# Optimization experiments

Measured on AMD Instinct MI355X. Metric: run time of the kernel, lower is better.

The kernel has to match this reference:

```python
import jax, jax.numpy as jnp
import numpy as np

N_NODES = 50000
N_EDGES = 800000
IN_F = 512
H_F = 32
HEADS = 8
N_CLS = 40
NEG_SLOPE = 0.2


def gat_conv(h, W, al, ar, b, src, dst, n_heads, d_out):
    """DGL-style GATConv. h: [N, F_in]; W: [F_in, n_heads*d_out];
    al, ar: [n_heads, d_out]; b: [n_heads*d_out]. Returns [N, n_heads, d_out]."""
    n = h.shape[0]
    feat = (h @ W).reshape(n, n_heads, d_out)            # [N, H, D]
    el = jnp.sum(feat * al[None], axis=-1)               # [N, H]
    er = jnp.sum(feat * ar[None], axis=-1)               # [N, H]
    e = jax.nn.leaky_relu(el[src] + er[dst], NEG_SLOPE)  # [E, H]
    # numerically stable edge softmax per destination node
    m = jax.ops.segment_max(e, dst, num_segments=n)      # [N, H]
    m = jnp.where(jnp.isfinite(m), m, 0.0)
    ee = jnp.exp(e - m[dst])                             # [E, H]
    den = jax.ops.segment_sum(ee, dst, num_segments=n)   # [N, H]
    alpha = ee / jnp.maximum(den[dst], 1e-9)             # [E, H]
    msg = alpha[:, :, None] * feat[src]                  # [E, H, D]
    rst = jax.ops.segment_sum(msg, dst, num_segments=n)  # [N, H, D]
    return rst + b.reshape(1, n_heads, d_out)


def setup_inputs() -> dict:
    key = jax.random.key(0)
    ks = jax.random.split(key, 16)
    hid = H_F * HEADS
    s = lambda fan: 1.0 / np.sqrt(fan)
    return {
        "in_feat": jax.random.normal(ks[0], (N_NODES, IN_F), jnp.float32),
        "src": jax.random.randint(ks[1], (N_EDGES,), 0, N_NODES, jnp.int32),
        "dst": jax.random.randint(ks[2], (N_EDGES,), 0, N_NODES, jnp.int32),
        "W0": jax.random.normal(ks[3], (IN_F, hid), jnp.float32) * s(IN_F),
        "al0": jax.random.normal(ks[4], (HEADS, H_F), jnp.float32) * s(H_F),
        "ar0": jax.random.normal(ks[5], (HEADS, H_F), jnp.float32) * s(H_F),
        "b0": jnp.zeros((hid,), jnp.float32),
        "W1": jax.random.normal(ks[6], (hid, hid), jnp.float32) * s(hid),
        "al1": jax.random.normal(ks[7], (HEADS, H_F), jnp.float32) * s(H_F),
        "ar1": jax.random.normal(ks[8], (HEADS, H_F), jnp.float32) * s(H_F),
        "b1": jnp.zeros((hid,), jnp.float32),
        "W2": jax.random.normal(ks[9], (hid, N_CLS), jnp.float32) * s(hid),
        "al2": jax.random.normal(ks[10], (1, N_CLS), jnp.float32) * s(N_CLS),
        "ar2": jax.random.normal(ks[11], (1, N_CLS), jnp.float32) * s(N_CLS),
        "b2": jnp.zeros((N_CLS,), jnp.float32),
    }


def reference(in_feat, src, dst, W0, al0, ar0, b0, W1, al1, ar1, b1,
              W2, al2, ar2, b2):
    n = in_feat.shape[0]
    # layer 0 + ReLU (dropout p=0.0 is identity) + flatten heads
    h = gat_conv(in_feat, W0, al0, ar0, b0, src, dst, HEADS, H_F)
    h = jax.nn.relu(h).reshape(n, -1)
    # layer 1
    h = gat_conv(h, W1, al1, ar1, b1, src, dst, HEADS, H_F)
    h = jax.nn.relu(h).reshape(n, -1)
    # output layer, single head, no activation
    h = gat_conv(h, W2, al2, ar2, b2, src, dst, 1, N_CLS)
    return h.reshape(n, -1)
```

## Files before the change

kernel.cpp:

```cpp
#include <hip/hip_runtime.h>
#include <hip/hip_bf16.h>

#define N_NODES 50000
#define N_EDGES 800000
#define IN_F 512
#define HID 256
#define HEADS 8
#define DHEAD 32
#define N_CLS 40
#define NCLS_PAD 64

typedef __bf16 bf16x8 __attribute__((ext_vector_type(8)));
typedef float f32x4 __attribute__((ext_vector_type(4)));

#define AT_AL0 0
#define AT_AR0 256
#define AT_AL1 512
#define AT_AR1 768
#define AT_AL2 1024
#define AT_AR2 1088
#define AT_B0  1152
#define AT_B1  1408
#define AT_B2  1664
#define AT_SZ  1792

__device__ __forceinline__ float ldflag(const void* p, long long i, int isbf) {
  return isbf ? __bfloat162float(((const __hip_bfloat16*)p)[i])
              : ((const float*)p)[i];
}
__device__ __forceinline__ float blo(unsigned u) { return __uint_as_float(u << 16); }
__device__ __forceinline__ float bhi(unsigned u) { return __uint_as_float(u & 0xffff0000u); }
__device__ __forceinline__ unsigned pk2(float a, float b) {
  unsigned x = __bfloat16_as_ushort(__float2bfloat16(a));
  unsigned y = __bfloat16_as_ushort(__float2bfloat16(b));
  return x | (y << 16);
}
__device__ __forceinline__ void gload16(const unsigned short* g, unsigned short* l) {
  __builtin_amdgcn_global_load_lds((__attribute__((address_space(1))) void*)g,
                                   (__attribute__((address_space(3))) void*)l, 16, 0, 0);
}

__global__ void k_zero(int* __restrict__ cursor) {
  int i = blockIdx.x * blockDim.x + threadIdx.x;
  if (i < N_NODES) cursor[i] = 0;
}

__global__ void k_detect_prep(const unsigned short* __restrict__ raw, int* __restrict__ flag,
                              const void* al0, const void* ar0, const void* al1, const void* ar1,
                              const void* al2, const void* ar2, const void* b0, const void* b1,
                              const void* b2, float* __restrict__ att) {
  __shared__ int cnt[256];
  int t = threadIdx.x;
  int c = 0;
  for (int i = t; i < 8192; i += 256) {
    int e = (raw[i] >> 7) & 0xFF;
    if (e >= 0x90) c++;
  }
  cnt[t] = c;
  __syncthreads();
  for (int s = 128; s; s >>= 1) {
    if (t < s) cnt[t] += cnt[t + s];
    __syncthreads();
  }
  __shared__ int sflag;
  if (t == 0) { sflag = (cnt[0] > 64) ? 0 : 1; *flag = sflag; }
  __syncthreads();
  int isbf = sflag;
  att[AT_AL0 + t] = ldflag(al0, t, isbf);
  att[AT_AR0 + t] = ldflag(ar0, t, isbf);
  att[AT_AL1 + t] = ldflag(al1, t, isbf);
  att[AT_AR1 + t] = ldflag(ar1, t, isbf);
  att[AT_B0 + t]  = ldflag(b0, t, isbf);
  att[AT_B1 + t]  = ldflag(b1, t, isbf);
  if (t < N_CLS) {
    att[AT_AL2 + t] = ldflag(al2, t, isbf);
    att[AT_AR2 + t] = ldflag(ar2, t, isbf);
    att[AT_B2 + t]  = ldflag(b2, t, isbf);
  }
}

__global__ void k_hist(const int* __restrict__ dst, int* __restrict__ cnt) {
  int e = blockIdx.x * blockDim.x + threadIdx.x;
  if (e < N_EDGES) atomicAdd(&cnt[dst[e]], 1);
}

#define SCAN_B 512
#define SCAN_NB ((N_NODES + SCAN_B - 1) / SCAN_B)

__global__ __launch_bounds__(SCAN_B) void k_scan_blocks(const int* __restrict__ deg,
                                                        int* __restrict__ excl,
                                                        int* __restrict__ partial) {
  __shared__ int buf[SCAN_B];
  int t = threadIdx.x;
  int i = blockIdx.x * SCAN_B + t;
  int v = (i < N_NODES) ? deg[i] : 0;
  buf[t] = v;
  __syncthreads();
  for (int off = 1; off < SCAN_B; off <<= 1) {
    int x = (t >= off) ? buf[t - off] : 0;
    __syncthreads();
    buf[t] += x;
    __syncthreads();
  }
  if (i < N_NODES) excl[i] = buf[t] - v;
  if (t == SCAN_B - 1) partial[blockIdx.x] = buf[t];
}

__global__ void k_scan_partials(int* __restrict__ partial, int* __restrict__ rowptr) {
  __shared__ int buf[SCAN_NB];
  int t = threadIdx.x;
  if (t < SCAN_NB) buf[t] = partial[t];
  __syncthreads();
  if (t == 0) {
    int run = 0;
    for (int b = 0; b < SCAN_NB; b++) { int v = buf[b]; buf[b] = run; run += v; }
    rowptr[N_NODES] = run;
  }
  __syncthreads();
  if (t < SCAN_NB) partial[t] = buf[t];
}

__global__ void k_scan_add(int* __restrict__ rowptr, const int* __restrict__ partial,
                           int* __restrict__ cursor) {
  int i = blockIdx.x * blockDim.x + threadIdx.x;
  if (i < N_NODES) {
    rowptr[i] += partial[i / SCAN_B];
    cursor[i] = 0;
  }
}

__global__ void k_scatter(const int* __restrict__ src, const int* __restrict__ dst,
                          const int* __restrict__ rowptr, int* __restrict__ cursor,
                          int* __restrict__ csr_src) {
  int e = blockIdx.x * blockDim.x + threadIdx.x;
  if (e < N_EDGES) {
    int d = dst[e];
    int pos = rowptr[d] + atomicAdd(&cursor[d], 1);
    csr_src[pos] = src[e];
  }
}

#define TW0 (HID * IN_F)
#define TW1 (TW0 + HID * HID)
#define TW2 (TW1 + NCLS_PAD * HID)
__global__ void k_transpose_all(const void* __restrict__ W0, const void* __restrict__ W1,
                                const void* __restrict__ W2,
                                __hip_bfloat16* __restrict__ w0t, __hip_bfloat16* __restrict__ w1t,
                                __hip_bfloat16* __restrict__ w2t, const int* __restrict__ flag) {
  int isbf = *flag;
  int i = blockIdx.x * blockDim.x + threadIdx.x;
  if (i < TW0) {
    int n = i >> 9, k = i & 511;
    w0t[i] = __float2bfloat16(ldflag(W0, (long long)k * HID + n, isbf));
  } else if (i < TW1) {
    int j = i - TW0;
    int n = j >> 8, k = j & 255;
    w1t[j] = __float2bfloat16(ldflag(W1, (long long)k * HID + n, isbf));
  } else if (i < TW2) {
    int j = i - TW1;
    int n = j >> 8, k = j & 255;
    float v = (n < N_CLS) ? ldflag(W2, (long long)k * N_CLS + n, isbf) : 0.f;
    w2t[j] = __float2bfloat16(v);
  }
}

__global__ __launch_bounds__(256, 8) void k_gemm64hi(const void* __restrict__ A,
                                                     const __hip_bfloat16* __restrict__ Bt,
                                                     __hip_bfloat16* __restrict__ C,
                                                     int M, int K, int N, int ldc, int nvalid,
                                                     const int* __restrict__ flag, int force_bf,
                                                     const float* __restrict__ al,
                                                     const float* __restrict__ ar,
                                                     float* __restrict__ el,
                                                     float* __restrict__ er, int fuse_eler) {
  __shared__ unsigned short sA[64 * 64];
  __shared__ unsigned short sB[64 * 64];
  const int isbf = force_bf ? 1 : *flag;
  int nwg = gridDim.x;
  int q = nwg >> 3, r = nwg & 7;
  int xcd = blockIdx.x & 7, lid = blockIdx.x >> 3;
  int logical = (xcd < r ? xcd * (q + 1) : r * (q + 1) + (xcd - r) * q) + lid;
  int nblk = N >> 6;
  int mb = logical / nblk;
  int nb = logical - mb * nblk;
  int m0 = mb << 6, n0 = nb << 6;
  int tid = threadIdx.x;
  int lane = tid & 63, wave = tid >> 6;
  int wm = (wave >> 1) << 5, wn = (wave & 1) << 5;
  int lm = lane & 15, quad = lane >> 4;
  int rbase = tid >> 3;
  int srcoff = ((tid & 7) ^ (rbase & 7)) << 3;
  const unsigned short* Ab = (const unsigned short*)A;
  const float* Af = (const float*)A;
  const unsigned short* Bb = (const unsigned short*)Bt;
  size_t abase[2];
  size_t bbase[2];
  #pragma unroll
  for (int i = 0; i < 2; i++) {
    int row = (i << 5) + rbase;
    int ga = m0 + row; if (ga > M - 1) ga = M - 1;
    abase[i] = (size_t)ga * K + srcoff;
    bbase[i] = (size_t)(n0 + row) * K + srcoff;
  }
  f32x4 acc[2][2] = {};
  int nph = K >> 6;
  for (int p = 0; p < nph; ++p) {
    int kph = p << 6;
    if (isbf) {
      #pragma unroll
      for (int i = 0; i < 2; i++) {
        gload16(Ab + abase[i] + kph, &sA[(((i << 8) + tid) << 3)]);
        gload16(Bb + bbase[i] + kph, &sB[(((i << 8) + tid) << 3)]);
      }
    } else {
      #pragma unroll
      for (int i = 0; i < 2; i++) {
        gload16(Bb + bbase[i] + kph, &sB[(((i << 8) + tid) << 3)]);
        const float* p0 = Af + abase[i] + kph;
        float4 x = *(const float4*)p0;
        float4 y = *(const float4*)(p0 + 4);
        *(uint4*)&sA[(((i << 8) + tid) << 3)] =
            make_uint4(pk2(x.x, x.y), pk2(x.z, x.w), pk2(y.x, y.y), pk2(y.z, y.w));
      }
    }
    __syncthreads();
    #pragma unroll
    for (int s = 0; s < 2; s++) {
      bf16x8 af[2], bfr[2];
      #pragma unroll
      for (int i = 0; i < 2; i++) {
        int ra = wm + (i << 4) + lm;
        int rb = wn + (i << 4) + lm;
        int sl = (((s << 2) + quad) ^ (lm & 7)) << 3;
        af[i]  = *(const bf16x8*)&sA[(ra << 6) + sl];
        bfr[i] = *(const bf16x8*)&sB[(rb << 6) + sl];
      }
      #pragma unroll
      for (int mi = 0; mi < 2; mi++)
        #pragma unroll
        for (int ni = 0; ni < 2; ni++)
          acc[mi][ni] = __builtin_amdgcn_mfma_f32_16x16x32_bf16(af[mi], bfr[ni], acc[mi][ni], 0, 0, 0);
    }
    __syncthreads();
  }
  #pragma unroll
  for (int mi = 0; mi < 2; mi++)
    #pragma unroll
    for (int ni = 0; ni < 2; ni++)
      #pragma unroll
      for (int r2 = 0; r2 < 4; r2++) {
        int gm = m0 + wm + mi * 16 + (quad << 2) + r2;
        int gn = n0 + wn + ni * 16 + lm;
        if (gm < M && gn < nvalid) C[(size_t)gm * ldc + gn] = __float2bfloat16(acc[mi][ni][r2]);
      }
  if (fuse_eler) {
    int hg = (n0 + wn) >> 5;
    float ala[2], ara[2];
    #pragma unroll
    for (int ni = 0; ni < 2; ni++) {
      ala[ni] = al[hg * DHEAD + ni * 16 + lm];
      ara[ni] = ar[hg * DHEAD + ni * 16 + lm];
    }
    #pragma unroll
    for (int mi = 0; mi < 2; mi++)
      #pragma unroll
      for (int r2 = 0; r2 < 4; r2++) {
        float pl = acc[mi][0][r2] * ala[0] + acc[mi][1][r2] * ala[1];
        float pr = acc[mi][0][r2] * ara[0] + acc[mi][1][r2] * ara[1];
        #pragma unroll
        for (int d = 1; d < 16; d <<= 1) {
          pl += __shfl_xor(pl, d, 16);
          pr += __shfl_xor(pr, d, 16);
        }
        int gm = m0 + wm + mi * 16 + (quad << 2) + r2;
        if (lm == 0 && gm < M) {
          el[gm * HEADS + hg] = pl;
          er[gm * HEADS + hg] = pr;
        }
      }
  }
}

__global__ void k_eler2(const __hip_bfloat16* __restrict__ feat2,
                        const float* __restrict__ al, const float* __restrict__ ar,
                        float* __restrict__ el, float* __restrict__ er) {
  int n = blockIdx.x * blockDim.x + threadIdx.x;
  if (n >= N_NODES) return;
  const __hip_bfloat16* f = feat2 + (size_t)n * N_CLS;
  float sl = 0.f, sr = 0.f;
  for (int d = 0; d < N_CLS; d++) {
    float v = __bfloat162float(f[d]);
    sl += v * al[d];
    sr += v * ar[d];
  }
  el[n] = sl;
  er[n] = sr;
}

__global__ __launch_bounds__(256) void k_aggregate8(const int* __restrict__ rowptr,
                                                    const int* __restrict__ csr_src,
                                                    const uint4* __restrict__ feat_rows,
                                                    const float* __restrict__ el,
                                                    const float* __restrict__ er,
                                                    const float* __restrict__ bias,
                                                    __hip_bfloat16* __restrict__ out) {
  __shared__ float lds_acc[8][256];
  __shared__ float lds_l[8][32];
  int n = blockIdx.x;
  int t = threadIdx.x;
  int slot = t >> 5;
  int c = t & 31;
  int hh = c >> 2;
  float er_n = er[n * HEADS + hh];
  int beg = rowptr[n], end = rowptr[n + 1];
  float l = 0.f;
  float acc[8] = {0.f, 0.f, 0.f, 0.f, 0.f, 0.f, 0.f, 0.f};
  int i = beg + slot;
  for (; i + 8 < end; i += 16) {
    int s1 = csr_src[i];
    int s2 = csr_src[i + 8];
    float el1 = el[s1 * HEADS + hh];
    float el2 = el[s2 * HEADS + hh];
    uint4 f1 = feat_rows[(size_t)s1 * 32 + c];
    uint4 f2 = feat_rows[(size_t)s2 * 32 + c];
    float x1 = el1 + er_n, x2 = el2 + er_n;
    float e1 = x1 > 0.f ? x1 : 0.2f * x1;
    float e2 = x2 > 0.f ? x2 : 0.2f * x2;
    float p1 = __expf(fminf(e1, 60.f));
    float p2 = __expf(fminf(e2, 60.f));
    l += p1 + p2;
    acc[0] += p1 * blo(f1.x) + p2 * blo(f2.x); acc[1] += p1 * bhi(f1.x) + p2 * bhi(f2.x);
    acc[2] += p1 * blo(f1.y) + p2 * blo(f2.y); acc[3] += p1 * bhi(f1.y) + p2 * bhi(f2.y);
    acc[4] += p1 * blo(f1.z) + p2 * blo(f2.z); acc[5] += p1 * bhi(f1.z) + p2 * bhi(f2.z);
    acc[6] += p1 * blo(f1.w) + p2 * blo(f2.w); acc[7] += p1 * bhi(f1.w) + p2 * bhi(f2.w);
  }
  if (i < end) {
    int s = csr_src[i];
    float elv = el[s * HEADS + hh];
    uint4 fv = feat_rows[(size_t)s * 32 + c];
    float x = elv + er_n;
    float e = x > 0.f ? x : 0.2f * x;
    float p = __expf(fminf(e, 60.f));
    l += p;
    acc[0] += p * blo(fv.x); acc[1] += p * bhi(fv.x);
    acc[2] += p * blo(fv.y); acc[3] += p * bhi(fv.y);
    acc[4] += p * blo(fv.z); acc[5] += p * bhi(fv.z);
    acc[6] += p * blo(fv.w); acc[7] += p * bhi(fv.w);
  }
  *(float4*)&lds_acc[slot][c * 8]     = make_float4(acc[0], acc[1], acc[2], acc[3]);
  *(float4*)&lds_acc[slot][c * 8 + 4] = make_float4(acc[4], acc[5], acc[6], acc[7]);
  lds_l[slot][c] = l;
  __syncthreads();
  float a = 0.f, L = 0.f;
  #pragma unroll
  for (int s2 = 0; s2 < 8; s2++) { a += lds_acc[s2][t]; L += lds_l[s2][t >> 3]; }
  float o = a / fmaxf(L, 1e-9f) + bias[t];
  o = fmaxf(o, 0.f);
  out[(size_t)n * HID + t] = __float2bfloat16(o);
}

__global__ __launch_bounds__(256) void k_aggregate1(const int* __restrict__ rowptr,
                                                    const int* __restrict__ csr_src,
                                                    const char* __restrict__ fr2,
                                                    const float* __restrict__ el,
                                                    const float* __restrict__ er,
                                                    const float* __restrict__ bias,
                                                    void* __restrict__ out,
                                                    const int* __restrict__ flag) {
  __shared__ float lds_acc[32][64];
  __shared__ float lds_l[32][8];
  int isbf = *flag;
  int n = blockIdx.x;
  int t = threadIdx.x;
  int slot = t >> 3;
  int c = t & 7;
  int beg = rowptr[n], end = rowptr[n + 1];
  if (c < 5) {
    float er_n = er[n];
    float l = 0.f;
    float acc[8] = {0.f, 0.f, 0.f, 0.f, 0.f, 0.f, 0.f, 0.f};
    unsigned cb = (unsigned)c << 4;
    int i = beg + slot;
    for (; i + 32 < end; i += 64) {
      int s1 = csr_src[i], s2 = csr_src[i + 32];
      float el1 = el[s1], el2 = el[s2];
      uint4 f1 = *(const uint4*)(fr2 + (unsigned)s1 * 80u + cb);
      uint4 f2 = *(const uint4*)(fr2 + (unsigned)s2 * 80u + cb);
      float x1 = el1 + er_n, x2 = el2 + er_n;
      float e1 = x1 > 0.f ? x1 : 0.2f * x1;
      float e2 = x2 > 0.f ? x2 : 0.2f * x2;
      float p1 = __expf(fminf(e1, 60.f));
      float p2 = __expf(fminf(e2, 60.f));
      l += p1 + p2;
      acc[0] += p1 * blo(f1.x) + p2 * blo(f2.x); acc[1] += p1 * bhi(f1.x) + p2 * bhi(f2.x);
      acc[2] += p1 * blo(f1.y) + p2 * blo(f2.y); acc[3] += p1 * bhi(f1.y) + p2 * bhi(f2.y);
      acc[4] += p1 * blo(f1.z) + p2 * blo(f2.z); acc[5] += p1 * bhi(f1.z) + p2 * bhi(f2.z);
      acc[6] += p1 * blo(f1.w) + p2 * blo(f2.w); acc[7] += p1 * bhi(f1.w) + p2 * bhi(f2.w);
    }
    if (i < end) {
      int s = csr_src[i];
      float x = el[s] + er_n;
      uint4 fv = *(const uint4*)(fr2 + (unsigned)s * 80u + cb);
      float e = x > 0.f ? x : 0.2f * x;
      float p = __expf(fminf(e, 60.f));
      l += p;
      acc[0] += p * blo(fv.x); acc[1] += p * bhi(fv.x);
      acc[2] += p * blo(fv.y); acc[3] += p * bhi(fv.y);
      acc[4] += p * blo(fv.z); acc[5] += p * bhi(fv.z);
      acc[6] += p * blo(fv.w); acc[7] += p * bhi(fv.w);
    }
    *(float4*)&lds_acc[slot][c * 8]     = make_float4(acc[0], acc[1], acc[2], acc[3]);
    *(float4*)&lds_acc[slot][c * 8 + 4] = make_float4(acc[4], acc[5], acc[6], acc[7]);
    lds_l[slot][c] = l;
  }
  __syncthreads();
  if (t < N_CLS) {
    float a = 0.f, L = 0.f;
    #pragma unroll
    for (int s2 = 0; s2 < 32; s2++) { a += lds_acc[s2][t]; L += lds_l[s2][t >> 3]; }
    float o = a / fmaxf(L, 1e-9f) + bias[t];
    if (isbf) ((__hip_bfloat16*)out)[(size_t)n * N_CLS + t] = __float2bfloat16(o);
    else      ((float*)out)[(size_t)n * N_CLS + t] = o;
  }
}

static inline size_t align_up(size_t x) { return (x + 255) & ~(size_t)255; }

extern "C" void kernel_launch(void* const* d_in, const int* in_sizes, int n_in,
                              void* d_out, int out_size, void* d_ws, size_t ws_size,
                              hipStream_t stream) {
  const void* in_feat = d_in[0];
  const int* src = (const int*)d_in[1];
  const int* dst = (const int*)d_in[2];
  const void* W0  = d_in[3];
  const void* al0 = d_in[4];
  const void* ar0 = d_in[5];
  const void* b0  = d_in[6];
  const void* W1  = d_in[7];
  const void* al1 = d_in[8];
  const void* ar1 = d_in[9];
  const void* b1  = d_in[10];
  const void* W2  = d_in[11];
  const void* al2 = d_in[12];
  const void* ar2 = d_in[13];
  const void* b2  = d_in[14];

  char* p = (char*)d_ws;
  int* flag = (int*)p;                   p += 256;
  float* att = (float*)p;                p += align_up(AT_SZ * sizeof(float));
  int* rowptr = (int*)p;                 p += align_up((N_NODES + 1) * sizeof(int));
  int* cursor = (int*)p;                 p += align_up(N_NODES * sizeof(int));
  int* csr_src = (int*)p;                p += align_up(N_EDGES * sizeof(int));
  int* partial = (int*)p;                p += align_up(SCAN_NB * sizeof(int));
  __hip_bfloat16* feat16 = (__hip_bfloat16*)p; p += align_up((size_t)N_NODES * HID * sizeof(__hip_bfloat16));
  __hip_bfloat16* h16 = (__hip_bfloat16*)p;    p += align_up((size_t)N_NODES * HID * sizeof(__hip_bfloat16));
  float* el = (float*)p;                 p += align_up((size_t)N_NODES * HEADS * sizeof(float));
  float* er = (float*)p;                 p += align_up((size_t)N_NODES * HEADS * sizeof(float));
  __hip_bfloat16* w0t = (__hip_bfloat16*)p;    p += align_up((size_t)HID * IN_F * sizeof(__hip_bfloat16));
  __hip_bfloat16* w1t = (__hip_bfloat16*)p;    p += align_up((size_t)HID * HID * sizeof(__hip_bfloat16));
  __hip_bfloat16* w2t = (__hip_bfloat16*)p;    p += align_up((size_t)NCLS_PAD * HID * sizeof(__hip_bfloat16));

  const int EB = (N_EDGES + 255) / 256;
  const int NB256 = (N_NODES + 255) / 256;
  const int MB64 = (N_NODES + 63) / 64;
  const int GXL = MB64 * 4;
  const int GX2 = MB64;

  k_detect_prep<<<1, 256, 0, stream>>>((const unsigned short*)in_feat, flag,
                                       al0, ar0, al1, ar1, al2, ar2, b0, b1, b2, att);
  k_zero<<<NB256, 256, 0, stream>>>(cursor);

  k_hist<<<EB, 256, 0, stream>>>(dst, cursor);
  k_scan_blocks<<<SCAN_NB, SCAN_B, 0, stream>>>(cursor, rowptr, partial);
  k_scan_partials<<<1, 128, 0, stream>>>(partial, rowptr);
  k_scan_add<<<NB256, 256, 0, stream>>>(rowptr, partial, cursor);
  k_scatter<<<EB, 256, 0, stream>>>(src, dst, rowptr, cursor, csr_src);

  k_transpose_all<<<(TW2 + 255) / 256, 256, 0, stream>>>(W0, W1, W2, w0t, w1t, w2t, flag);

  k_gemm64hi<<<GXL, 256, 0, stream>>>(in_feat, w0t, feat16, N_NODES, IN_F, HID, HID, HID, flag, 0,
                                      att + AT_AL0, att + AT_AR0, el, er, 1);
  k_aggregate8<<<N_NODES, 256, 0, stream>>>(rowptr, csr_src, (const uint4*)feat16, el, er, att + AT_B0, h16);

  k_gemm64hi<<<GXL, 256, 0, stream>>>(h16, w1t, feat16, N_NODES, HID, HID, HID, HID, flag, 1,
                                      att + AT_AL1, att + AT_AR1, el, er, 1);
  k_aggregate8<<<N_NODES, 256, 0, stream>>>(rowptr, csr_src, (const uint4*)feat16, el, er, att + AT_B1, h16);

  k_gemm64hi<<<GX2, 256, 0, stream>>>(h16, w2t, feat16, N_NODES, HID, NCLS_PAD, N_CLS, N_CLS, flag, 1,
                                      nullptr, nullptr, nullptr, nullptr, 0);
  k_eler2<<<NB256, 256, 0, stream>>>(feat16, att + AT_AL2, att + AT_AR2, el, er);
  k_aggregate1<<<N_NODES, 256, 0, stream>>>(rowptr, csr_src, (const char*)feat16, el, er, att + AT_B2, d_out, flag);
}
```

Before: 524.0 us.

## Store hidden features head-major and aggregate per head with one node per 4 lanes

The GEMM epilogue for the hidden layers now writes features and el/er in a head-major layout ([head][node][32] and [head][node]). The aggregation kernel is rewritten so each block handles one head for 64 nodes, with 4 lanes per node walking that node's edge list serially. This drops the LDS reduction and the __syncthreads. The aim is better cache locality, since each head's feature table (about 3.2 MB) is small enough to stay cache-resident during random gathers. The trade-off is per-lane serial edge loops, which can leave lanes idle when node degrees differ.

```diff
diff --git a/kernel.cpp b/kernel.cpp
--- a/kernel.cpp
+++ b/kernel.cpp
@@ -243,18 +243,19 @@
     }
     __syncthreads();
   }
-  #pragma unroll
-  for (int mi = 0; mi < 2; mi++)
+  if (fuse_eler) {
+    int hg = (n0 + wn) >> 5;
     #pragma unroll
-    for (int ni = 0; ni < 2; ni++)
+    for (int mi = 0; mi < 2; mi++)
       #pragma unroll
       for (int r2 = 0; r2 < 4; r2++) {
         int gm = m0 + wm + mi * 16 + (quad << 2) + r2;
-        int gn = n0 + wn + ni * 16 + lm;
-        if (gm < M && gn < nvalid) C[(size_t)gm * ldc + gn] = __float2bfloat16(acc[mi][ni][r2]);
+        if (gm < M) {
+          #pragma unroll
+          for (int ni = 0; ni < 2; ni++)
+            C[(((size_t)hg * M + gm) << 5) + (ni << 4) + lm] = __float2bfloat16(acc[mi][ni][r2]);
+        }
       }
-  if (fuse_eler) {
-    int hg = (n0 + wn) >> 5;
     float ala[2], ara[2];
     #pragma unroll
     for (int ni = 0; ni < 2; ni++) {
@@ -274,10 +275,21 @@
         }
         int gm = m0 + wm + mi * 16 + (quad << 2) + r2;
         if (lm == 0 && gm < M) {
-          el[gm * HEADS + hg] = pl;
-          er[gm * HEADS + hg] = pr;
+          el[(size_t)hg * M + gm] = pl;
+          er[(size_t)hg * M + gm] = pr;
         }
       }
+  } else {
+    #pragma unroll
+    for (int mi = 0; mi < 2; mi++)
+      #pragma unroll
+      for (int ni = 0; ni < 2; ni++)
+        #pragma unroll
+        for (int r2 = 0; r2 < 4; r2++) {
+          int gm = m0 + wm + mi * 16 + (quad << 2) + r2;
+          int gn = n0 + wn + ni * 16 + lm;
+          if (gm < M && gn < nvalid) C[(size_t)gm * ldc + gn] = __float2bfloat16(acc[mi][ni][r2]);
+        }
   }
 }
 
@@ -297,33 +309,35 @@
   er[n] = sr;
 }
 
-__global__ __launch_bounds__(256) void k_aggregate8(const int* __restrict__ rowptr,
-                                                    const int* __restrict__ csr_src,
-                                                    const uint4* __restrict__ feat_rows,
-                                                    const float* __restrict__ el,
-                                                    const float* __restrict__ er,
-                                                    const float* __restrict__ bias,
-                                                    __hip_bfloat16* __restrict__ out) {
-  __shared__ float lds_acc[8][256];
-  __shared__ float lds_l[8][32];
-  int n = blockIdx.x;
-  int t = threadIdx.x;
-  int slot = t >> 5;
-  int c = t & 31;
-  int hh = c >> 2;
-  float er_n = er[n * HEADS + hh];
+__global__ __launch_bounds__(256) void k_aggregate_h(const int* __restrict__ rowptr,
+                                                     const int* __restrict__ csr_src,
+                                                     const uint4* __restrict__ feat_h,
+                                                     const float* __restrict__ el_h,
+                                                     const float* __restrict__ er_h,
+                                                     const float* __restrict__ bias,
+                                                     __hip_bfloat16* __restrict__ out) {
+  int h = blockIdx.x & 7;
+  int grp = blockIdx.x >> 3;
+  int tid = threadIdx.x;
+  int lane = tid & 63, wave = tid >> 6;
+  int dloc = lane >> 2;
+  int chunk = lane & 3;
+  int n = grp * 64 + wave * 16 + dloc;
+  if (n >= N_NODES) return;
+  const uint4* fh = feat_h + (size_t)h * N_NODES * 4;
+  const float* elh = el_h + (size_t)h * N_NODES;
+  float er_n = er_h[(size_t)h * N_NODES + n];
   int beg = rowptr[n], end = rowptr[n + 1];
   float l = 0.f;
   float acc[8] = {0.f, 0.f, 0.f, 0.f, 0.f, 0.f, 0.f, 0.f};
-  int i = beg + slot;
-  for (; i + 8 < end; i += 16) {
+  int i = beg;
+  for (; i + 1 < end; i += 2) {
     int s1 = csr_src[i];
-    int s2 = csr_src[i + 8];
-    float el1 = el[s1 * HEADS + hh];
-    float el2 = el[s2 * HEADS + hh];
-    uint4 f1 = feat_rows[(size_t)s1 * 32 + c];
-    uint4 f2 = feat_rows[(size_t)s2 * 32 + c];
-    float x1 = el1 + er_n, x2 = el2 + er_n;
+    int s2 = csr_src[i + 1];
+    float x1 = elh[s1] + er_n;
+    float x2 = elh[s2] + er_n;
+    uint4 f1 = fh[(size_t)s1 * 4 + chunk];
+    uint4 f2 = fh[(size_t)s2 * 4 + chunk];
     float e1 = x1 > 0.f ? x1 : 0.2f * x1;
     float e2 = x2 > 0.f ? x2 : 0.2f * x2;
     float p1 = __expf(fminf(e1, 60.f));
@@ -336,9 +350,8 @@
   }
   if (i < end) {
     int s = csr_src[i];
-    float elv = el[s * HEADS + hh];
-    uint4 fv = feat_rows[(size_t)s * 32 + c];
-    float x = elv + er_n;
+    float x = elh[s] + er_n;
+    uint4 fv = fh[(size_t)s * 4 + chunk];
     float e = x > 0.f ? x : 0.2f * x;
     float p = __expf(fminf(e, 60.f));
     l += p;
@@ -347,16 +360,13 @@
     acc[4] += p * blo(fv.z); acc[5] += p * bhi(fv.z);
     acc[6] += p * blo(fv.w); acc[7] += p * bhi(fv.w);
   }
-  *(float4*)&lds_acc[slot][c * 8]     = make_float4(acc[0], acc[1], acc[2], acc[3]);
-  *(float4*)&lds_acc[slot][c * 8 + 4] = make_float4(acc[4], acc[5], acc[6], acc[7]);
-  lds_l[slot][c] = l;
-  __syncthreads();
-  float a = 0.f, L = 0.f;
+  float inv = 1.f / fmaxf(l, 1e-9f);
+  const float* bp = bias + h * 32 + chunk * 8;
+  float o[8];
   #pragma unroll
-  for (int s2 = 0; s2 < 8; s2++) { a += lds_acc[s2][t]; L += lds_l[s2][t >> 3]; }
-  float o = a / fmaxf(L, 1e-9f) + bias[t];
-  o = fmaxf(o, 0.f);
-  out[(size_t)n * HID + t] = __float2bfloat16(o);
+  for (int j = 0; j < 8; j++) o[j] = fmaxf(acc[j] * inv + bp[j], 0.f);
+  __hip_bfloat16* op = out + (size_t)n * HID + h * 32 + chunk * 8;
+  *(uint4*)op = make_uint4(pk2(o[0], o[1]), pk2(o[2], o[3]), pk2(o[4], o[5]), pk2(o[6], o[7]));
 }
 
 __global__ __launch_bounds__(256) void k_aggregate1(const int* __restrict__ rowptr,
@@ -465,6 +475,7 @@
   const int MB64 = (N_NODES + 63) / 64;
   const int GXL = MB64 * 4;
   const int GX2 = MB64;
+  const int GAH = MB64 * 8;
 
   k_detect_prep<<<1, 256, 0, stream>>>((const unsigned short*)in_feat, flag,
                                        al0, ar0, al1, ar1, al2, ar2, b0, b1, b2, att);
@@ -480,11 +491,13 @@
 
   k_gemm64hi<<<GXL, 256, 0, stream>>>(in_feat, w0t, feat16, N_NODES, IN_F, HID, HID, HID, flag, 0,
                                       att + AT_AL0, att + AT_AR0, el, er, 1);
-  k_aggregate8<<<N_NODES, 256, 0, stream>>>(rowptr, csr_src, (const uint4*)feat16, el, er, att + AT_B0, h16);
+  k_aggregate_h<<<GAH, 256, 0, stream>>>(rowptr, csr_src, (const uint4*)feat16, el, er,
+                                         att + AT_B0, h16);
 
   k_gemm64hi<<<GXL, 256, 0, stream>>>(h16, w1t, feat16, N_NODES, HID, HID, HID, HID, flag, 1,
                                       att + AT_AL1, att + AT_AR1, el, er, 1);
-  k_aggregate8<<<N_NODES, 256, 0, stream>>>(rowptr, csr_src, (const uint4*)feat16, el, er, att + AT_B1, h16);
+  k_aggregate_h<<<GAH, 256, 0, stream>>>(rowptr, csr_src, (const uint4*)feat16, el, er,
+                                         att + AT_B1, h16);
 
   k_gemm64hi<<<GX2, 256, 0, stream>>>(h16, w2t, feat16, N_NODES, HID, NCLS_PAD, N_CLS, N_CLS, flag, 1,
                                       nullptr, nullptr, nullptr, nullptr, 0);
```

Measured after the change: 536.6 us. +2.4%, slower.
